# Kernel tuning notes

Measured on AMD Instinct MI355X. Metric: run time of the kernel, lower is better.

Reference implementation:

```python
import jax, jax.numpy as jnp
import numpy as np

B, T, N = 1, 1024, 8
D_S, D_R, H, TOPK = 1024, 512, 8, 4
DH_S, DH_R = D_S // H, D_R // H
EPS = 1e-6


def _rmsnorm(x, w):
    return x * jax.lax.rsqrt(jnp.mean(x * x, axis=-1, keepdims=True) + EPS) * w


def setup_inputs() -> dict:
    key = jax.random.key(0)
    ks = jax.random.split(key, 12)

    def lin(k, fan_in, fan_out):
        b = 1.0 / np.sqrt(fan_in)
        return jax.random.uniform(k, (fan_in, fan_out), jnp.float32, -b, b)

    return {
        "s": jax.random.normal(ks[0], (B, T, D_S), jnp.float32),
        "r": jax.random.normal(ks[1], (B, T, N, D_R), jnp.float32),
        "gate_v": jax.random.uniform(ks[2], (B, T, 1), dtype=jnp.float32),
        "norm_s_w": jnp.ones((D_S,), jnp.float32),
        "norm_r_w": jnp.ones((D_R,), jnp.float32),
        "Wsq": lin(ks[3], D_S, D_S),
        "Wsk": lin(ks[4], D_R, D_S),
        "Wsv": lin(ks[5], D_R, D_S),
        "Wso": lin(ks[6], D_S, D_S),
        "Wrq": lin(ks[7], D_R, D_R),
        "Wrk": lin(ks[8], D_S, D_R),
        "Wrv": lin(ks[9], D_S, D_R),
        "Wro": lin(ks[10], D_R, D_R),
    }


def reference(s, r, gate_v, norm_s_w, norm_r_w, Wsq, Wsk, Wsv, Wso, Wrq, Wrk, Wrv, Wro):
    scale_s = DH_S ** -0.5
    scale_r = DH_R ** -0.5
    s_n = _rmsnorm(s, norm_s_w)  # (B,T,D_S)
    r_n = _rmsnorm(r, norm_r_w)  # (B,T,N,D_R)

    # --- s reads its own prefix-local reasoning slots (_s_reads_prefix_r) ---
    q = (s_n @ Wsq).reshape(B, T, H, DH_S)
    k = (r_n @ Wsk).reshape(B, T, N, H, DH_S)
    v = (r_n @ Wsv).reshape(B, T, N, H, DH_S)
    w = jax.nn.softmax(jnp.einsum('bthd,btnhd->bthn', q, k) * scale_s, axis=-1)
    s2 = s + jnp.einsum('bthn,btnhd->bthd', w, v).reshape(B, T, D_S) @ Wso

    # --- reasoning slots attend causally over surface prefix (_r_reads_s_causal) ---
    qr = (r_n @ Wrq).reshape(B, T, N, H, DH_R)
    kr = (s_n @ Wrk).reshape(B, T, H, DH_R)
    vr = (s_n @ Wrv).reshape(B, T, H, DH_R)
    scores = jnp.einsum('btnhd,bphd->btnhp', qr, kr) * scale_r  # (B,T,N,H,T)
    causal = jnp.arange(T)[:, None] >= jnp.arange(T)[None, :]  # p <= t
    scores = jnp.where(causal[None, :, None, None, :], scores, -jnp.inf)
    wr = jax.nn.softmax(scores, axis=-1)
    r2 = r + jnp.einsum('btnhp,bphd->btnhd', wr, vr).reshape(B, T, N, D_R) @ Wro

    # --- sparse top-k prefix write-back (_sparse_prefix_r_to_s) ---
    qs = s_n @ Wsq                       # (B,T,D_S)
    ksp = r_n @ Wsk                      # (B,T,N,D_S)
    vsp = r_n @ Wsv                      # (B,T,N,D_S)
    sp = jnp.einsum('btd,btnd->btn', qs, ksp) * scale_s
    vals, idx = jax.lax.top_k(sp, TOPK)
    wk = jax.nn.softmax(vals, axis=-1)   # softmax over scattered -inf == softmax over top-k
    onehot = jax.nn.one_hot(idx, N, dtype=sp.dtype)  # (B,T,K,N)
    weights = jnp.einsum('btk,btkn->btn', wk, onehot)
    r_sparse = jnp.einsum('btn,btnd->btd', weights, vsp)

    return (s2 + gate_v * r_sparse, r2)
```

## Files before the change

### kernel.cpp

```cpp
#include <hip/hip_runtime.h>
#include <hip/hip_bf16.h>
#include <math.h>
#include <type_traits>


#define T_DIM 1024
#define N_SLOT 8
#define DS 1024
#define DR 512
#define NH 8
#define DHS 128
#define DHR 64

typedef __attribute__((ext_vector_type(8))) short short8v;
typedef __attribute__((ext_vector_type(4))) float floatx4;

#define GLDS(gptr, lptr)                                                     \
  __builtin_amdgcn_global_load_lds(                                          \
      (__attribute__((address_space(1))) void*)(gptr),                       \
      (__attribute__((address_space(3))) void*)(lptr), 16, 0, 0)

struct TJob { const float* W; __hip_bfloat16* Wt; int K; int N; float scale; int b0; };
struct TJobs { TJob j[8]; };

__global__ __launch_bounds__(256) void prep_kernel(
    TJobs jobs, const float* __restrict__ s, const float* __restrict__ r,
    const float* __restrict__ nsw, const float* __restrict__ nrw,
    __hip_bfloat16* __restrict__ s_nb, float* __restrict__ s_n32,
    __hip_bfloat16* __restrict__ r_nb) {
  __shared__ float sh[32][33];
  const int tid = threadIdx.x;
  if (blockIdx.x < 4608) {
    int ji = 0;
#pragma unroll
    for (int t = 1; t < 8; ++t)
      if ((int)blockIdx.x >= jobs.j[t].b0) ji = t;
    const TJob J = jobs.j[ji];
    const int lb = blockIdx.x - J.b0;
    const int nbx = J.N >> 5;
    const int n0 = (lb % nbx) * 32, k0 = (lb / nbx) * 32;
    const int tx = tid & 31, ty = tid >> 5;
#pragma unroll
    for (int i = 0; i < 4; ++i) {
      int kk = ty + i * 8;
      sh[kk][tx] = J.W[(size_t)(k0 + kk) * J.N + n0 + tx];
    }
    __syncthreads();
#pragma unroll
    for (int i = 0; i < 4; ++i) {
      int nn = ty + i * 8;
      J.Wt[(size_t)(n0 + nn) * J.K + k0 + tx] = __float2bfloat16(sh[tx][nn] * J.scale);
    }
  } else {
    const int blk = blockIdx.x - 4608;
    const bool is_s = blk < 1024;
    const int row = is_s ? blk : blk - 1024;
    const int width = is_s ? DS : DR;
    const float* x = is_s ? s : r;
    const float* w = is_s ? nsw : nrw;
    const size_t base = (size_t)row * width;
    float ss = 0.f;
    for (int i = tid; i < width; i += 256) {
      float v = x[base + i];
      ss += v * v;
    }
    for (int m = 32; m >= 1; m >>= 1) ss += __shfl_xor(ss, m);
    const int wave = tid >> 6, lane = tid & 63;
    if (lane == 0) sh[0][wave] = ss;
    __syncthreads();
    float total = sh[0][0] + sh[0][1] + sh[0][2] + sh[0][3];
    float scale = rsqrtf(total / (float)width + 1e-6f);
    for (int i = tid; i < width; i += 256) {
      float val = x[base + i] * scale * w[i];
      if (is_s) {
        s_nb[base + i] = __float2bfloat16(val);
        s_n32[base + i] = val;
      } else {
        r_nb[base + i] = __float2bfloat16(val);
      }
    }
  }
}

template <int BS, int TT, bool BT, bool BSUM>
__global__ __launch_bounds__(256) void gemm_f32_kernel(
    const float* __restrict__ A, const float* __restrict__ B,
    float* __restrict__ C, int M, int N, int K) {
  __shared__ __align__(16) float Ast[16][BS + 4];
  __shared__ __align__(16) float Bs[16][BS + 4];
  const int tid = threadIdx.x;
  const int tx = tid & 15, ty = tid >> 4;
  const int row0 = blockIdx.y * BS, col0 = blockIdx.x * BS;
  const int kz = blockIdx.z;
  const int kbeg = kz * (K >> 1), kend = kbeg + (K >> 1);
  float* Cz = C + (size_t)kz * M * N;
  const size_t bsz = (size_t)K * N;
  float acc[TT][TT] = {};
  constexpr int NF4 = BS * 16 / 4;
  for (int k0 = kbeg; k0 < kend; k0 += 16) {
    __syncthreads();
    for (int l = tid; l < NF4; l += 256) {
      int lr = l >> 2, lk = (l & 3) << 2;
      float4 a4 = *(const float4*)&A[(size_t)(row0 + lr) * K + k0 + lk];
      Ast[lk + 0][lr] = a4.x;
      Ast[lk + 1][lr] = a4.y;
      Ast[lk + 2][lr] = a4.z;
      Ast[lk + 3][lr] = a4.w;
      if (BT) {
        float4 b4 = *(const float4*)&B[(size_t)(col0 + lr) * K + k0 + lk];
        Bs[lk + 0][lr] = b4.x;
        Bs[lk + 1][lr] = b4.y;
        Bs[lk + 2][lr] = b4.z;
        Bs[lk + 3][lr] = b4.w;
      } else {
        int bkk = l / (BS / 4), bc = (l % (BS / 4)) << 2;
        size_t bidx = (size_t)(k0 + bkk) * N + col0 + bc;
        float4 b4 = *(const float4*)&B[bidx];
        if (BSUM) {
          float4 b2 = *(const float4*)&B[bsz + bidx];
          b4.x += b2.x; b4.y += b2.y; b4.z += b2.z; b4.w += b2.w;
        }
        *(float4*)&Bs[bkk][bc] = b4;
      }
    }
    __syncthreads();
#pragma unroll
    for (int kk = 0; kk < 16; ++kk) {
      float av[TT], bv[TT];
#pragma unroll
      for (int u = 0; u < TT; u += 4) {
        *(float4*)&av[u] = *(const float4*)&Ast[kk][ty * TT + u];
        *(float4*)&bv[u] = *(const float4*)&Bs[kk][tx * TT + u];
      }
#pragma unroll
      for (int i = 0; i < TT; ++i)
#pragma unroll
        for (int j = 0; j < TT; ++j) acc[i][j] += av[i] * bv[j];
    }
  }
#pragma unroll
  for (int i = 0; i < TT; ++i) {
    size_t crow = (size_t)(row0 + ty * TT + i) * N + col0;
#pragma unroll
    for (int j = 0; j < TT; j += 4) {
      *(float4*)&Cz[crow + tx * TT + j] =
          make_float4(acc[i][j], acc[i][j + 1], acc[i][j + 2], acc[i][j + 3]);
    }
  }
}

template <int MT, bool ACCUM, typename OutT, bool RADD = false>
__global__ __launch_bounds__(256) void mfma_gemm_kernel(
    const __hip_bfloat16* __restrict__ A, const __hip_bfloat16* __restrict__ Bt,
    OutT* __restrict__ C, const float* __restrict__ R, int M, int N, int K) {
  constexpr int FR = MT / 32;
  constexpr int HALF = MT / 2;
  constexpr int SEG_PER_WAVE = MT / 16 / 4;
  __shared__ __hip_bfloat16 As[MT][32];
  __shared__ __hip_bfloat16 Bs[MT][32];
  const int tid = threadIdx.x;
  const int lane = tid & 63, wave = tid >> 6;
  const int wm = wave >> 1, wn = wave & 1;
  const int l15 = lane & 15, l4 = lane >> 4;
  const int row0 = blockIdx.y * MT, col0 = blockIdx.x * MT;
  const int dma_r = lane >> 2;
  const int dma_c = (lane & 3) ^ ((lane >> 3) & 3);
  const int rd_sw = (l15 >> 1) & 3;
  floatx4 acc[FR][FR] = {};
  for (int k0 = 0; k0 < K; k0 += 32) {
    __syncthreads();
#pragma unroll
    for (int i = 0; i < SEG_PER_WAVE; ++i) {
      int seg = wave * SEG_PER_WAVE + i;
      GLDS(&A[(size_t)(row0 + seg * 16 + dma_r) * K + k0 + dma_c * 8], &As[seg * 16][0]);
      GLDS(&Bt[(size_t)(col0 + seg * 16 + dma_r) * K + k0 + dma_c * 8], &Bs[seg * 16][0]);
    }
    __syncthreads();
    short8v af[FR], bf[FR];
#pragma unroll
    for (int i = 0; i < FR; ++i)
      af[i] = *(const short8v*)&As[wm * HALF + i * 16 + l15][(l4 ^ rd_sw) * 8];
#pragma unroll
    for (int j = 0; j < FR; ++j)
      bf[j] = *(const short8v*)&Bs[wn * HALF + j * 16 + l15][(l4 ^ rd_sw) * 8];
#pragma unroll
    for (int i = 0; i < FR; ++i)
#pragma unroll
      for (int j = 0; j < FR; ++j)
        acc[i][j] = __builtin_amdgcn_mfma_f32_16x16x32_bf16(af[i], bf[j], acc[i][j], 0, 0, 0);
  }
#pragma unroll
  for (int i = 0; i < FR; ++i) {
    int rb = row0 + wm * HALF + i * 16 + l4 * 4;
#pragma unroll
    for (int j = 0; j < FR; ++j) {
      int cb = col0 + wn * HALF + j * 16 + l15;
#pragma unroll
      for (int rg = 0; rg < 4; ++rg) {
        size_t idx = (size_t)(rb + rg) * N + cb;
        if constexpr (std::is_same<OutT, __hip_bfloat16>::value) {
          C[idx] = __float2bfloat16(acc[i][j][rg]);
        } else if constexpr (RADD) {
          C[idx] = R[idx] + acc[i][j][rg];
        } else if constexpr (ACCUM) {
          C[idx] += acc[i][j][rg];
        } else {
          C[idx] = acc[i][j][rg];
        }
      }
    }
  }
}

struct GJob { const __hip_bfloat16* Bt; __hip_bfloat16* C; int N; int b0; int trans; };
struct GJobs { GJob j[3]; };

template <int MT>
__global__ __launch_bounds__(256) void mfma_gemm_batch_kernel(
    const __hip_bfloat16* __restrict__ A, GJobs jobs, int M, int K) {
  constexpr int FR = MT / 32;
  constexpr int HALF = MT / 2;
  constexpr int SEG_PER_WAVE = MT / 16 / 4;
  __shared__ __hip_bfloat16 As[MT][32];
  __shared__ __hip_bfloat16 Bs[MT][32];
  int ji = 0;
#pragma unroll
  for (int t = 1; t < 3; ++t)
    if ((int)blockIdx.x >= jobs.j[t].b0) ji = t;
  const GJob J = jobs.j[ji];
  const int lb = blockIdx.x - J.b0;
  const int nbx = J.N / MT;
  const int row0 = (lb / nbx) * MT, col0 = (lb % nbx) * MT;
  const int tid = threadIdx.x;
  const int lane = tid & 63, wave = tid >> 6;
  const int wm = wave >> 1, wn = wave & 1;
  const int l15 = lane & 15, l4 = lane >> 4;
  const int dma_r = lane >> 2;
  const int dma_c = (lane & 3) ^ ((lane >> 3) & 3);
  const int rd_sw = (l15 >> 1) & 3;
  floatx4 acc[FR][FR] = {};
  for (int k0 = 0; k0 < K; k0 += 32) {
    __syncthreads();
#pragma unroll
    for (int i = 0; i < SEG_PER_WAVE; ++i) {
      int seg = wave * SEG_PER_WAVE + i;
      GLDS(&A[(size_t)(row0 + seg * 16 + dma_r) * K + k0 + dma_c * 8], &As[seg * 16][0]);
      GLDS(&J.Bt[(size_t)(col0 + seg * 16 + dma_r) * K + k0 + dma_c * 8], &Bs[seg * 16][0]);
    }
    __syncthreads();
    short8v af[FR], bf[FR];
#pragma unroll
    for (int i = 0; i < FR; ++i)
      af[i] = *(const short8v*)&As[wm * HALF + i * 16 + l15][(l4 ^ rd_sw) * 8];
#pragma unroll
    for (int j = 0; j < FR; ++j)
      bf[j] = *(const short8v*)&Bs[wn * HALF + j * 16 + l15][(l4 ^ rd_sw) * 8];
#pragma unroll
    for (int i = 0; i < FR; ++i)
#pragma unroll
      for (int j = 0; j < FR; ++j)
        acc[i][j] = __builtin_amdgcn_mfma_f32_16x16x32_bf16(af[i], bf[j], acc[i][j], 0, 0, 0);
  }
#pragma unroll
  for (int i = 0; i < FR; ++i) {
    int rb = row0 + wm * HALF + i * 16 + l4 * 4;
#pragma unroll
    for (int j = 0; j < FR; ++j) {
      int cb = col0 + wn * HALF + j * 16 + l15;
      if (J.trans) {
        __hip_bfloat16 pk[4];
#pragma unroll
        for (int rg = 0; rg < 4; ++rg) pk[rg] = __float2bfloat16(acc[i][j][rg]);
        *(ushort4*)&J.C[(size_t)cb * M + rb] = *(const ushort4*)pk;
      } else {
#pragma unroll
        for (int rg = 0; rg < 4; ++rg)
          J.C[(size_t)(rb + rg) * J.N + cb] = __float2bfloat16(acc[i][j][rg]);
      }
    }
  }
}

__global__ __launch_bounds__(256) void part1_kernel(
    const float* __restrict__ s, const float* __restrict__ gv,
    const __hip_bfloat16* __restrict__ q, const __hip_bfloat16* __restrict__ k,
    const __hip_bfloat16* __restrict__ v, const float* __restrict__ r,
    const float* __restrict__ nrw, const float* __restrict__ u0,
    const float* __restrict__ u1, __hip_bfloat16* __restrict__ attn1,
    float* __restrict__ outS) {
  __shared__ float qs[DS];
  __shared__ float dots[NH][N_SLOT];
  __shared__ float wattn[NH][N_SLOT];
  __shared__ float w8[N_SLOT];
  __shared__ float spv[N_SLOT];
  __shared__ float gateL;
  const int t = blockIdx.x;
  const int tid = threadIdx.x;
  for (int i = tid; i < DS; i += 256) qs[i] = __bfloat162float(q[(size_t)t * DS + i]);
  __syncthreads();
  const int wave = tid >> 6, lane = tid & 63;
#pragma unroll
  for (int e = 0; e < 16; ++e) {
    int pair = wave * 16 + e;
    int h = pair >> 3, n = pair & 7;
    const __hip_bfloat16* krow = &k[((size_t)t * N_SLOT + n) * DS + h * DHS];
    float a = qs[h * DHS + lane] * __bfloat162float(krow[lane]) +
              qs[h * DHS + 64 + lane] * __bfloat162float(krow[64 + lane]);
    for (int m = 32; m >= 1; m >>= 1) a += __shfl_xor(a, m);
    if (lane == 0) dots[h][n] = a;
  }
  const float scale_s = 0.08838834764831845f;
#pragma unroll
  for (int e = 0; e < 2; ++e) {
    const int n = wave * 2 + e;
    const float* rr = &r[((size_t)t * N_SLOT + n) * DR];
    const float* ub0 = &u0[(size_t)t * DR];
    const float* ub1 = &u1[(size_t)t * DR];
    float ssum = 0.f, dot = 0.f;
#pragma unroll
    for (int jj = 0; jj < 8; ++jj) {
      int j = lane + 64 * jj;
      float rv = rr[j];
      ssum += rv * rv;
      dot += rv * nrw[j] * (ub0[j] + ub1[j]);
    }
    for (int m = 32; m >= 1; m >>= 1) {
      ssum += __shfl_xor(ssum, m);
      dot += __shfl_xor(dot, m);
    }
    if (lane == 0) {
      float rs = rsqrtf(ssum / (float)DR + 1e-6f);
      spv[n] = scale_s * rs * dot;
    }
  }
  __syncthreads();
  if (tid < 8) {
    int h = tid;
    float vmax = -1e30f;
    for (int n = 0; n < 8; ++n) vmax = fmaxf(vmax, dots[h][n] * scale_s);
    float sum = 0.f;
    for (int n = 0; n < 8; ++n) {
      float e = __expf(dots[h][n] * scale_s - vmax);
      wattn[h][n] = e;
      sum += e;
    }
    float inv = 1.f / sum;
    for (int n = 0; n < 8; ++n) wattn[h][n] *= inv;
  }
  if (tid == 64) {
    float sv[8];
    for (int n = 0; n < 8; ++n) sv[n] = spv[n];
    bool used[8] = {};
    float vals[4];
    int idxs[4];
    for (int kk = 0; kk < 4; ++kk) {
      float best = -1e30f;
      int bi = 0;
      for (int n = 0; n < 8; ++n)
        if (!used[n] && sv[n] > best) { best = sv[n]; bi = n; }
      used[bi] = true;
      vals[kk] = best;
      idxs[kk] = bi;
    }
    float mx = vals[0];
    float wv[4];
    float sum = 0.f;
    for (int kk = 0; kk < 4; ++kk) {
      wv[kk] = __expf(vals[kk] - mx);
      sum += wv[kk];
    }
    float inv = 1.f / sum;
    for (int n = 0; n < 8; ++n) w8[n] = 0.f;
    for (int kk = 0; kk < 4; ++kk) w8[idxs[kk]] = wv[kk] * inv;
    gateL = gv[t];
  }
  __syncthreads();
  const float gate = gateL;
#pragma unroll
  for (int jj = 0; jj < 4; ++jj) {
    int d = tid + 256 * jj;
    int hh = d >> 7;
    float a1 = 0.f, a2 = 0.f;
#pragma unroll
    for (int n = 0; n < 8; ++n) {
      float vv = __bfloat162float(v[((size_t)t * N_SLOT + n) * DS + d]);
      a1 += wattn[hh][n] * vv;
      a2 += w8[n] * vv;
    }
    attn1[(size_t)t * DS + d] = __float2bfloat16(a1);
    outS[(size_t)t * DS + d] = s[(size_t)t * DS + d] + gate * a2;
  }
}

__global__ __launch_bounds__(256) void flash_mfma_kernel(
    const __hip_bfloat16* __restrict__ qb, const __hip_bfloat16* __restrict__ kb,
    const __hip_bfloat16* __restrict__ vbT, __hip_bfloat16* __restrict__ rat) {
  __shared__ __align__(16) __hip_bfloat16 Qs[64][72];
  __shared__ __align__(16) __hip_bfloat16 Ks[64][72];
  __shared__ __align__(16) __hip_bfloat16 Vt[64][72];
  __shared__ __align__(16) __hip_bfloat16 Pb[64][72];
  const int tid = threadIdx.x;
  const int lane = tid & 63, wave = tid >> 6;
  const int l15 = lane & 15, l4 = lane >> 4;
  const int h = blockIdx.y;
  const int qbase = blockIdx.x * 64;
  const int s = wave * 16;

  for (int g = tid; g < 512; g += 256) {
    int rr = g >> 3, c = (g & 7) * 8;
    *(ulonglong2*)&Qs[rr][c] =
        *(const ulonglong2*)&qb[(size_t)(qbase + rr) * DR + h * DHR + c];
  }
  __syncthreads();
  short8v qf[2];
#pragma unroll
  for (int kk = 0; kk < 2; ++kk)
    qf[kk] = *(const short8v*)&Qs[s + l15][kk * 32 + l4 * 8];

  const int myt = (qbase + s + l15) >> 3;
  const int tmin = (qbase + s) >> 3;
  const int tmax = (qbase + s + 15) >> 3;

  float m_r = -1e30f, l_r = 0.f;
  floatx4 o[4] = {};

  const int ntiles = (((qbase + 63) >> 3) >> 6) + 1;
  for (int pt = 0; pt < ntiles; ++pt) {
    const int p0 = pt << 6;
    __syncthreads();
    for (int g = tid; g < 512; g += 256) {
      int rr = g >> 3, c = (g & 7) * 8;
      *(ulonglong2*)&Ks[rr][c] =
          *(const ulonglong2*)&kb[(size_t)(p0 + rr) * DR + h * DHR + c];
      *(ulonglong2*)&Vt[rr][c] =
          *(const ulonglong2*)&vbT[(size_t)(h * DHR + rr) * T_DIM + p0 + c];
    }
    __syncthreads();
    if (p0 > tmax) continue;
    floatx4 sc[4] = {};
#pragma unroll
    for (int j = 0; j < 4; ++j)
#pragma unroll
      for (int kk = 0; kk < 2; ++kk) {
        short8v kf = *(const short8v*)&Ks[j * 16 + l15][kk * 32 + l4 * 8];
        sc[j] = __builtin_amdgcn_mfma_f32_16x16x32_bf16(kf, qf[kk], sc[j], 0, 0, 0);
      }
    if (p0 + 63 > tmin) {
#pragma unroll
      for (int j = 0; j < 4; ++j)
#pragma unroll
        for (int rg = 0; rg < 4; ++rg)
          if (p0 + j * 16 + l4 * 4 + rg > myt) sc[j][rg] = -1e30f;
    }
    float mx = m_r;
#pragma unroll
    for (int j = 0; j < 4; ++j)
#pragma unroll
      for (int rg = 0; rg < 4; ++rg) mx = fmaxf(mx, sc[j][rg]);
    mx = fmaxf(mx, __shfl_xor(mx, 16));
    mx = fmaxf(mx, __shfl_xor(mx, 32));
    float sum = 0.f;
#pragma unroll
    for (int j = 0; j < 4; ++j)
#pragma unroll
      for (int rg = 0; rg < 4; ++rg) {
        float e = __expf(sc[j][rg] - mx);
        sc[j][rg] = e;
        sum += e;
      }
    sum += __shfl_xor(sum, 16);
    sum += __shfl_xor(sum, 32);
    const float alpha = __expf(m_r - mx);
    l_r = alpha * l_r + sum;
    m_r = mx;
#pragma unroll
    for (int j = 0; j < 4; ++j) {
      __hip_bfloat16 pk[4];
#pragma unroll
      for (int rg = 0; rg < 4; ++rg) pk[rg] = __float2bfloat16(sc[j][rg]);
      *(ushort4*)&Pb[s + l15][j * 16 + l4 * 4] = *(const ushort4*)pk;
    }
#pragma unroll
    for (int jd = 0; jd < 4; ++jd) o[jd] *= alpha;
#pragma unroll
    for (int kk = 0; kk < 2; ++kk) {
      short8v pf = *(const short8v*)&Pb[s + l15][kk * 32 + l4 * 8];
#pragma unroll
      for (int jd = 0; jd < 4; ++jd) {
        short8v vf = *(const short8v*)&Vt[jd * 16 + l15][kk * 32 + l4 * 8];
        o[jd] = __builtin_amdgcn_mfma_f32_16x16x32_bf16(vf, pf, o[jd], 0, 0, 0);
      }
    }
  }
  const float inv = 1.f / l_r;
  const size_t rbase = (size_t)(qbase + s + l15) * DR + h * DHR;
#pragma unroll
  for (int jd = 0; jd < 4; ++jd) {
    __hip_bfloat16 pk[4];
#pragma unroll
    for (int rg = 0; rg < 4; ++rg) pk[rg] = __float2bfloat16(o[jd][rg] * inv);
    *(ushort4*)&rat[rbase + jd * 16 + l4 * 4] = *(const ushort4*)pk;
  }
}

extern "C" void kernel_launch(void* const* d_in, const int* in_sizes, int n_in,
                              void* d_out, int out_size, void* d_ws,
                              size_t ws_size, hipStream_t stream) {
  const float* s   = (const float*)d_in[0];
  const float* r   = (const float*)d_in[1];
  const float* gv  = (const float*)d_in[2];
  const float* nsw = (const float*)d_in[3];
  const float* nrw = (const float*)d_in[4];
  const float* Wsq = (const float*)d_in[5];
  const float* Wsk = (const float*)d_in[6];
  const float* Wsv = (const float*)d_in[7];
  const float* Wso = (const float*)d_in[8];
  const float* Wrq = (const float*)d_in[9];
  const float* Wrk = (const float*)d_in[10];
  const float* Wrv = (const float*)d_in[11];
  const float* Wro = (const float*)d_in[12];

  float* outS = (float*)d_out;
  float* outR = outS + 1048576;

  char* wp = (char*)d_ws;
  float* qreg = (float*)wp;           wp += 1048576 * 4;
  __hip_bfloat16* k   = (__hip_bfloat16*)wp; wp += 8388608 * 2;
  __hip_bfloat16* v   = (__hip_bfloat16*)wp; wp += 8388608 * 2;
  __hip_bfloat16* qrb = (__hip_bfloat16*)wp; wp += 4194304 * 2;
  __hip_bfloat16* krb = (__hip_bfloat16*)wp; wp += 524288 * 2;
  __hip_bfloat16* vrbT = (__hip_bfloat16*)wp; wp += 524288 * 2;
  __hip_bfloat16* s_nb = (__hip_bfloat16*)wp; wp += 1048576 * 2;
  __hip_bfloat16* r_nb = (__hip_bfloat16*)wp; wp += 4194304 * 2;
  __hip_bfloat16* WsqT = (__hip_bfloat16*)wp; wp += 1048576 * 2;
  __hip_bfloat16* WskT = (__hip_bfloat16*)wp; wp += 524288 * 2;
  __hip_bfloat16* WsvT = (__hip_bfloat16*)wp; wp += 524288 * 2;
  __hip_bfloat16* WsoT = (__hip_bfloat16*)wp; wp += 1048576 * 2;
  __hip_bfloat16* WrqT = (__hip_bfloat16*)wp; wp += 262144 * 2;
  __hip_bfloat16* WrkT = (__hip_bfloat16*)wp; wp += 524288 * 2;
  __hip_bfloat16* WrvT = (__hip_bfloat16*)wp; wp += 524288 * 2;
  __hip_bfloat16* WroT = (__hip_bfloat16*)wp; wp += 262144 * 2;

  float* s_n32 = qreg;
  __hip_bfloat16* q = (__hip_bfloat16*)qreg;
  float* Wc01 = (float*)r_nb;
  float* u0   = (float*)((char*)r_nb + 4194304);
  float* u1   = (float*)((char*)r_nb + 6291456);
  __hip_bfloat16* attn1b = s_nb;
  __hip_bfloat16* ratb   = r_nb;

  TJobs jobs = {{
      {Wsq, WsqT, 1024, 1024, 1.f, 0},
      {Wsk, WskT, 512, 1024, 1.f, 1024},
      {Wsv, WsvT, 512, 1024, 1.f, 1536},
      {Wso, WsoT, 1024, 1024, 1.f, 2048},
      {Wrq, WrqT, 512, 512, 0.125f, 3072},
      {Wrk, WrkT, 1024, 512, 1.f, 3328},
      {Wrv, WrvT, 1024, 512, 1.f, 3840},
      {Wro, WroT, 512, 512, 1.f, 4352},
  }};
  prep_kernel<<<13824, 256, 0, stream>>>(jobs, s, r, nsw, nrw, s_nb, s_n32, r_nb);

  GJobs ga = {{
      {WskT, k, 1024, 0, 0},
      {WsvT, v, 1024, 512, 0},
      {WrqT, qrb, 512, 1024, 0},
  }};
  mfma_gemm_batch_kernel<128><<<1280, 256, 0, stream>>>(r_nb, ga, 8192, 512);

  gemm_f32_kernel<64, 4, true, false><<<dim3(8, 16, 2), 256, 0, stream>>>(Wsq, Wsk, Wc01, 1024, 512, 1024);

  gemm_f32_kernel<64, 4, false, true><<<dim3(8, 16, 2), 256, 0, stream>>>(s_n32, Wc01, u0, 1024, 512, 1024);

  GJobs gb = {{
      {WsqT, q, 1024, 0, 0},
      {WrkT, krb, 512, 256, 0},
      {WrvT, vrbT, 512, 384, 1},
  }};
  mfma_gemm_batch_kernel<64><<<512, 256, 0, stream>>>(s_nb, gb, 1024, 1024);

  part1_kernel<<<1024, 256, 0, stream>>>(s, gv, q, k, v, r, nrw, u0, u1, attn1b, outS);

  mfma_gemm_kernel<64, true, float><<<dim3(16, 16), 256, 0, stream>>>(attn1b, WsoT, outS, nullptr, 1024, 1024, 1024);

  flash_mfma_kernel<<<dim3(128, 8), 256, 0, stream>>>(qrb, krb, vrbT, ratb);

  mfma_gemm_kernel<128, false, float, true><<<dim3(4, 64), 256, 0, stream>>>(ratb, WroT, outR, r, 8192, 512, 512);
}
```

Before: 321.7 us.

## Swizzle GEMM blocks across XCDs, vectorize bf16 loads, alias flash LDS buffers

GEMM kernels now remap a flattened block index so consecutive tiles land on the same XCD, aiming for better L2 reuse of shared A/B panels. part1_kernel reads bf16 q/k/v as packed 32-bit pairs and writes paired outputs, halving load/store instruction counts. The flash attention kernel reuses the Q staging buffer for P, shrinking LDS footprint and possibly raising occupancy. The Q reuse relies on qf being loaded into registers before the first P write.

```diff
diff --git a/kernel.cpp b/kernel.cpp
--- a/kernel.cpp
+++ b/kernel.cpp
@@ -19,6 +19,25 @@
   __builtin_amdgcn_global_load_lds(                                          \
       (__attribute__((address_space(1))) void*)(gptr),                       \
       (__attribute__((address_space(3))) void*)(lptr), 16, 0, 0)
+
+__device__ inline int xcd_swz(int b, int G) {
+  int per = G >> 3, rem = G & 7;
+  int x = b & 7, i = b >> 3;
+  return x * per + (x < rem ? x : rem) + i;
+}
+
+__device__ inline float bf_lo(unsigned int u) {
+  unsigned short x = (unsigned short)(u & 0xffff);
+  __hip_bfloat16 b;
+  __builtin_memcpy(&b, &x, 2);
+  return __bfloat162float(b);
+}
+__device__ inline float bf_hi(unsigned int u) {
+  unsigned short x = (unsigned short)(u >> 16);
+  __hip_bfloat16 b;
+  __builtin_memcpy(&b, &x, 2);
+  return __bfloat162float(b);
+}
 
 struct TJob { const float* W; __hip_bfloat16* Wt; int K; int N; float scale; int b0; };
 struct TJobs { TJob j[8]; };
@@ -152,17 +171,19 @@
 template <int MT, bool ACCUM, typename OutT, bool RADD = false>
 __global__ __launch_bounds__(256) void mfma_gemm_kernel(
     const __hip_bfloat16* __restrict__ A, const __hip_bfloat16* __restrict__ Bt,
-    OutT* __restrict__ C, const float* __restrict__ R, int M, int N, int K) {
+    OutT* __restrict__ C, const float* __restrict__ R, int M, int N, int K,
+    int nbx) {
   constexpr int FR = MT / 32;
   constexpr int HALF = MT / 2;
   constexpr int SEG_PER_WAVE = MT / 16 / 4;
   __shared__ __hip_bfloat16 As[MT][32];
   __shared__ __hip_bfloat16 Bs[MT][32];
+  const int sb = xcd_swz(blockIdx.x, gridDim.x);
+  const int row0 = (sb / nbx) * MT, col0 = (sb % nbx) * MT;
   const int tid = threadIdx.x;
   const int lane = tid & 63, wave = tid >> 6;
   const int wm = wave >> 1, wn = wave & 1;
   const int l15 = lane & 15, l4 = lane >> 4;
-  const int row0 = blockIdx.y * MT, col0 = blockIdx.x * MT;
   const int dma_r = lane >> 2;
   const int dma_c = (lane & 3) ^ ((lane >> 3) & 3);
   const int rd_sw = (l15 >> 1) & 3;
@@ -223,12 +244,13 @@
   constexpr int SEG_PER_WAVE = MT / 16 / 4;
   __shared__ __hip_bfloat16 As[MT][32];
   __shared__ __hip_bfloat16 Bs[MT][32];
+  const int sb = xcd_swz(blockIdx.x, gridDim.x);
   int ji = 0;
 #pragma unroll
   for (int t = 1; t < 3; ++t)
-    if ((int)blockIdx.x >= jobs.j[t].b0) ji = t;
+    if (sb >= jobs.j[t].b0) ji = t;
   const GJob J = jobs.j[ji];
-  const int lb = blockIdx.x - J.b0;
+  const int lb = sb - J.b0;
   const int nbx = J.N / MT;
   const int row0 = (lb / nbx) * MT, col0 = (lb % nbx) * MT;
   const int tid = threadIdx.x;
@@ -296,16 +318,25 @@
   __shared__ float gateL;
   const int t = blockIdx.x;
   const int tid = threadIdx.x;
-  for (int i = tid; i < DS; i += 256) qs[i] = __bfloat162float(q[(size_t)t * DS + i]);
+  {
+    const unsigned int* q2 = (const unsigned int*)&q[(size_t)t * DS];
+    for (int i = tid; i < DS / 2; i += 256) {
+      unsigned int pk = q2[i];
+      qs[2 * i] = bf_lo(pk);
+      qs[2 * i + 1] = bf_hi(pk);
+    }
+  }
   __syncthreads();
   const int wave = tid >> 6, lane = tid & 63;
 #pragma unroll
   for (int e = 0; e < 16; ++e) {
     int pair = wave * 16 + e;
     int h = pair >> 3, n = pair & 7;
-    const __hip_bfloat16* krow = &k[((size_t)t * N_SLOT + n) * DS + h * DHS];
-    float a = qs[h * DHS + lane] * __bfloat162float(krow[lane]) +
-              qs[h * DHS + 64 + lane] * __bfloat162float(krow[64 + lane]);
+    const unsigned int* kr2 =
+        (const unsigned int*)&k[((size_t)t * N_SLOT + n) * DS + h * DHS];
+    unsigned int pk = kr2[lane];
+    float a = qs[h * DHS + 2 * lane] * bf_lo(pk) +
+              qs[h * DHS + 2 * lane + 1] * bf_hi(pk);
     for (int m = 32; m >= 1; m >>= 1) a += __shfl_xor(a, m);
     if (lane == 0) dots[h][n] = a;
   }
@@ -377,28 +408,33 @@
   __syncthreads();
   const float gate = gateL;
 #pragma unroll
-  for (int jj = 0; jj < 4; ++jj) {
-    int d = tid + 256 * jj;
-    int hh = d >> 7;
-    float a1 = 0.f, a2 = 0.f;
+  for (int jj = 0; jj < 2; ++jj) {
+    int dp = tid + 256 * jj;
+    int hh = dp >> 6;
+    float a1x = 0.f, a1y = 0.f, a2x = 0.f, a2y = 0.f;
 #pragma unroll
     for (int n = 0; n < 8; ++n) {
-      float vv = __bfloat162float(v[((size_t)t * N_SLOT + n) * DS + d]);
-      a1 += wattn[hh][n] * vv;
-      a2 += w8[n] * vv;
-    }
-    attn1[(size_t)t * DS + d] = __float2bfloat16(a1);
-    outS[(size_t)t * DS + d] = s[(size_t)t * DS + d] + gate * a2;
+      unsigned int pv =
+          ((const unsigned int*)&v[((size_t)t * N_SLOT + n) * DS])[dp];
+      float vx = bf_lo(pv), vy = bf_hi(pv);
+      float wa = wattn[hh][n], wb = w8[n];
+      a1x += wa * vx; a1y += wa * vy;
+      a2x += wb * vx; a2y += wb * vy;
+    }
+    __hip_bfloat16 pk2[2] = {__float2bfloat16(a1x), __float2bfloat16(a1y)};
+    ((unsigned int*)&attn1[(size_t)t * DS])[dp] = *(const unsigned int*)pk2;
+    float2 sv = ((const float2*)&s[(size_t)t * DS])[dp];
+    ((float2*)&outS[(size_t)t * DS])[dp] =
+        make_float2(sv.x + gate * a2x, sv.y + gate * a2y);
   }
 }
 
 __global__ __launch_bounds__(256) void flash_mfma_kernel(
     const __hip_bfloat16* __restrict__ qb, const __hip_bfloat16* __restrict__ kb,
     const __hip_bfloat16* __restrict__ vbT, __hip_bfloat16* __restrict__ rat) {
-  __shared__ __align__(16) __hip_bfloat16 Qs[64][72];
+  __shared__ __align__(16) __hip_bfloat16 QP[64][72];
   __shared__ __align__(16) __hip_bfloat16 Ks[64][72];
   __shared__ __align__(16) __hip_bfloat16 Vt[64][72];
-  __shared__ __align__(16) __hip_bfloat16 Pb[64][72];
   const int tid = threadIdx.x;
   const int lane = tid & 63, wave = tid >> 6;
   const int l15 = lane & 15, l4 = lane >> 4;
@@ -408,14 +444,14 @@
 
   for (int g = tid; g < 512; g += 256) {
     int rr = g >> 3, c = (g & 7) * 8;
-    *(ulonglong2*)&Qs[rr][c] =
+    *(ulonglong2*)&QP[rr][c] =
         *(const ulonglong2*)&qb[(size_t)(qbase + rr) * DR + h * DHR + c];
   }
   __syncthreads();
   short8v qf[2];
 #pragma unroll
   for (int kk = 0; kk < 2; ++kk)
-    qf[kk] = *(const short8v*)&Qs[s + l15][kk * 32 + l4 * 8];
+    qf[kk] = *(const short8v*)&QP[s + l15][kk * 32 + l4 * 8];
 
   const int myt = (qbase + s + l15) >> 3;
   const int tmin = (qbase + s) >> 3;
@@ -478,13 +514,13 @@
       __hip_bfloat16 pk[4];
 #pragma unroll
       for (int rg = 0; rg < 4; ++rg) pk[rg] = __float2bfloat16(sc[j][rg]);
-      *(ushort4*)&Pb[s + l15][j * 16 + l4 * 4] = *(const ushort4*)pk;
+      *(ushort4*)&QP[s + l15][j * 16 + l4 * 4] = *(const ushort4*)pk;
     }
 #pragma unroll
     for (int jd = 0; jd < 4; ++jd) o[jd] *= alpha;
 #pragma unroll
     for (int kk = 0; kk < 2; ++kk) {
-      short8v pf = *(const short8v*)&Pb[s + l15][kk * 32 + l4 * 8];
+      short8v pf = *(const short8v*)&QP[s + l15][kk * 32 + l4 * 8];
 #pragma unroll
       for (int jd = 0; jd < 4; ++jd) {
         short8v vf = *(const short8v*)&Vt[jd * 16 + l15][kk * 32 + l4 * 8];
@@ -581,9 +617,9 @@
 
   part1_kernel<<<1024, 256, 0, stream>>>(s, gv, q, k, v, r, nrw, u0, u1, attn1b, outS);
 
-  mfma_gemm_kernel<64, true, float><<<dim3(16, 16), 256, 0, stream>>>(attn1b, WsoT, outS, nullptr, 1024, 1024, 1024);
+  mfma_gemm_kernel<64, true, float><<<256, 256, 0, stream>>>(attn1b, WsoT, outS, nullptr, 1024, 1024, 1024, 16);
 
   flash_mfma_kernel<<<dim3(128, 8), 256, 0, stream>>>(qrb, krb, vrbT, ratb);
 
-  mfma_gemm_kernel<128, false, float, true><<<dim3(4, 64), 256, 0, stream>>>(ratb, WroT, outR, r, 8192, 512, 512);
-}
+  mfma_gemm_kernel<128, false, float, true><<<256, 256, 0, stream>>>(ratb, WroT, outR, r, 8192, 512, 512, 4);
+}
```

Result: no change. 318.9 us (-0.9%).
